# Performance work log

Measured on AMD Instinct MI355X. Metric: run time of the kernel, lower is better.

Reference implementation:

```python
import jax, jax.numpy as jnp
import numpy as np

NUM_LAYERS = 2
VOCAB = 32000
IN_FEAT = 256          # embedding dim is IN_FEAT-1, +1 for cue scalar
HIDDEN = 256
ATN = 64               # hardcoded atn_feature_size in GraphConvolution
CLASSES = 2
B, N = 8, 2048


def setup_inputs() -> dict:
    key = jax.random.key(0)
    ks = jax.random.split(key, 12)
    x = jax.random.randint(ks[0], (B, N), 0, VOCAB, dtype=jnp.int32)
    cue = jax.random.randint(ks[1], (B, N), 0, 2, dtype=jnp.int32)
    adj = (jax.random.uniform(ks[2], (B, N, N)) < 0.01).astype(jnp.float32)
    s = 1.0 / np.sqrt(HIDDEN)
    emb_table = jax.random.normal(ks[3], (VOCAB, IN_FEAT - 1), jnp.float32) * 0.02
    Wh = jax.random.uniform(ks[4], (IN_FEAT, HIDDEN), jnp.float32, -s, s)
    bh = jax.random.uniform(ks[5], (HIDDEN,), jnp.float32, -s, s)
    Wq = jax.random.uniform(ks[6], (HIDDEN, ATN), jnp.float32, -s, s)
    Wk = jax.random.uniform(ks[7], (HIDDEN, ATN), jnp.float32, -s, s)
    Wv = jax.random.uniform(ks[8], (HIDDEN, HIDDEN), jnp.float32, -s, s)
    gcb = jax.random.uniform(ks[9], (HIDDEN,), jnp.float32, -s, s)
    Wc = jax.random.uniform(ks[10], (HIDDEN, CLASSES), jnp.float32, -s, s)
    bc = jax.random.uniform(ks[11], (CLASSES,), jnp.float32, -s, s)
    return {"x": x, "cue": cue, "adj": adj, "emb_table": emb_table,
            "Wh": Wh, "bh": bh, "Wq": Wq, "Wk": Wk, "Wv": Wv,
            "gcb": gcb, "Wc": Wc, "bc": bc}


def graph_attention_layer(h, adj, Wq, Wk, Wv, gcb):
    # h: [B,N,H]; adj: [B,N,N] binary. Per node i: softmax over neighbors j of
    # (Wk h_j) . (Wq h_i), weighted sum of Wv h_j. Zero-degree nodes get 0 (pre-bias).
    q = jnp.einsum('bnh,ha->bna', h, Wq)        # [B,N,A]
    k = jnp.einsum('bnh,ha->bna', h, Wk)        # [B,N,A]
    v = jnp.einsum('bnh,hg->bng', h, Wv)        # [B,N,H]
    logits = jnp.einsum('bia,bja->bij', q, k)   # [B,N,N]
    mask = adj > 0
    attn = jax.nn.softmax(jnp.where(mask, logits, -1e9), axis=-1)
    out = jnp.einsum('bij,bjh->bih', attn, v)   # [B,N,H]
    has_nbr = jnp.any(mask, axis=-1, keepdims=True)  # [B,N,1]
    return jnp.where(has_nbr, out, 0.0) + gcb


def reference(x, cue, adj, emb_table, Wh, bh, Wq, Wk, Wv, gcb, Wc, bc):
    emb = emb_table[x]                                   # [B,N,IN_FEAT-1]
    feats = jnp.concatenate([emb, cue.astype(jnp.float32)[..., None]], axis=-1)
    h = jax.nn.relu(jnp.einsum('bnf,fh->bnh', feats, Wh) + bh)
    for _ in range(NUM_LAYERS):
        h = jax.nn.sigmoid(graph_attention_layer(h, adj, Wq, Wk, Wv, gcb))
    logits = jnp.einsum('bnh,hc->bnc', h, Wc) + bc
    return jax.nn.softmax(logits, axis=-1)
```

## Files before the change

### kernel.cpp

```cpp
#include <hip/hip_runtime.h>
#include <hip/hip_bf16.h>


#define NB 8
#define NN 2048
#define ROWS (NB * NN)
#define MAXD 64

typedef float f4 __attribute__((ext_vector_type(4)));
typedef _Float16 hf;
typedef _Float16 h2 __attribute__((ext_vector_type(2)));
typedef _Float16 h4 __attribute__((ext_vector_type(4)));
typedef _Float16 h8 __attribute__((ext_vector_type(8)));
typedef unsigned int  u32;
typedef unsigned short u16;

__device__ __forceinline__ float sigmoidf_(float x) { return 1.f / (1.f + __expf(-x)); }
__device__ __forceinline__ h2 u2h(u32 u) { union { u32 u; h2 h; } c; c.u = u; return c.h; }

__device__ __forceinline__ float dot2_(h2 a, h2 b, float c) {
#if __has_builtin(__builtin_amdgcn_fdot2)
    return __builtin_amdgcn_fdot2(a, b, c, false);
#else
    return c + (float)a.x * (float)b.x + (float)a.y * (float)b.y;
#endif
}
__device__ __forceinline__ u32 permlo_(u32 hi, u32 lo) { return __builtin_amdgcn_perm(hi, lo, 0x05040100u); }
__device__ __forceinline__ u32 permhi_(u32 hi, u32 lo) { return __builtin_amdgcn_perm(hi, lo, 0x07060302u); }

#define PACK_BLKS 96
#define EMB_BLKS 512

__global__ __launch_bounds__(256) void k_fused_front(
        const int* __restrict__ x, const int* __restrict__ cue,
        const float* __restrict__ adj, const float* __restrict__ emb,
        const float* __restrict__ Wh, const float* __restrict__ bh,
        const float* __restrict__ Wq, const float* __restrict__ Wk,
        const float* __restrict__ Wv,
        hf* __restrict__ hB, hf* __restrict__ Wpt,
        int* __restrict__ deg, int* __restrict__ nbr) {
    __shared__ float As[32 * 64];
    __shared__ float Ws[32 * 128];
    int bid = blockIdx.x;
    int t = threadIdx.x;

    if (bid < PACK_BLKS) {
        int idxp = bid * 256 + t;
#pragma unroll
        for (int r = 0; r < 4; ++r) {
            int i = idxp + r * PACK_BLKS * 256;
            int c = i >> 8, f = i & 255;
            float v;
            if (c < 64)       v = Wq[f * 64 + c];
            else if (c < 128) v = Wk[f * 64 + (c - 64)];
            else              v = Wv[f * 256 + (c - 128)];
            Wpt[i] = (hf)v;
        }
        return;
    }

    if (bid < PACK_BLKS + EMB_BLKS) {
        int eb = bid - PACK_BLKS;
        int rt = eb >> 1, ct = eb & 1;
        int row0 = rt * 64, col0 = ct * 128;
        int sm = t & 63, skg = t >> 6;
        int swc = (t & 31) * 4, swk = t >> 5;
        int tx = t & 15, ty = t >> 4;
        int xr = x[row0 + sm];
        float cv = (float)cue[row0 + sm];
        const float* er = emb + (size_t)xr * 255;

        float acc[4][8];
#pragma unroll
        for (int i = 0; i < 4; ++i)
#pragma unroll
            for (int j = 0; j < 8; ++j) acc[i][j] = 0.f;

        for (int kc = 0; kc < 256; kc += 32) {
            int kb = skg * 8;
#pragma unroll
            for (int u = 0; u < 8; ++u) {
                int f = kc + kb + u;
                As[(kb + u) * 64 + sm] = (f < 255) ? er[f] : cv;
            }
#pragma unroll
            for (int r = 0; r < 4; ++r) {
                int kk = swk + r * 8;
                f4 w = *(const f4*)(Wh + (size_t)(kc + kk) * 256 + col0 + swc);
                *(f4*)&Ws[kk * 128 + swc] = w;
            }
            __syncthreads();
#pragma unroll
            for (int k = 0; k < 32; ++k) {
                f4 av = *(f4*)&As[k * 64 + ty * 4];
                f4 w0 = *(f4*)&Ws[k * 128 + tx * 8];
                f4 w1 = *(f4*)&Ws[k * 128 + tx * 8 + 4];
                float a[4] = {av.x, av.y, av.z, av.w};
                float w[8] = {w0.x, w0.y, w0.z, w0.w, w1.x, w1.y, w1.z, w1.w};
#pragma unroll
                for (int i = 0; i < 4; ++i)
#pragma unroll
                    for (int j = 0; j < 8; ++j) acc[i][j] += a[i] * w[j];
            }
            __syncthreads();
        }
        f4 b0 = *(const f4*)(bh + col0 + tx * 8);
        f4 b1 = *(const f4*)(bh + col0 + tx * 8 + 4);
        float bb[8] = {b0.x, b0.y, b0.z, b0.w, b1.x, b1.y, b1.z, b1.w};
#pragma unroll
        for (int i = 0; i < 4; ++i) {
            int row = row0 + ty * 4 + i;
            h8 o;
#pragma unroll
            for (int j = 0; j < 8; ++j) o[j] = (hf)fmaxf(acc[i][j] + bb[j], 0.f);
            *(h8*)(hB + (size_t)row * 256 + col0 + tx * 8) = o;
        }
        return;
    }

    int row = bid - (PACK_BLKS + EMB_BLKS);
    const f4* ar4 = (const f4*)(adj + (size_t)row * NN);
    int* cnt = (int*)As;
    if (t == 0) *cnt = 0;
    __syncthreads();
    int* nr = nbr + (size_t)row * MAXD;
#pragma unroll
    for (int it = 0; it < 2; ++it) {
        int idx = it * 256 + t;
        f4 vv = __builtin_nontemporal_load(ar4 + idx);
        if (vv.x > 0.f) { int p = atomicAdd(cnt, 1); if (p < MAXD) nr[p] = idx * 4 + 0; }
        if (vv.y > 0.f) { int p = atomicAdd(cnt, 1); if (p < MAXD) nr[p] = idx * 4 + 1; }
        if (vv.z > 0.f) { int p = atomicAdd(cnt, 1); if (p < MAXD) nr[p] = idx * 4 + 2; }
        if (vv.w > 0.f) { int p = atomicAdd(cnt, 1); if (p < MAXD) nr[p] = idx * 4 + 3; }
    }
    __syncthreads();
    if (t == 0) deg[row] = (*cnt < MAXD) ? *cnt : MAXD;
}

__global__ __launch_bounds__(256) void k_qkv_mfma(const hf* __restrict__ hB,
                                                  const hf* __restrict__ Wpt,
                                                  hf* __restrict__ qkvB) {
    int t = threadIdx.x;
    int col0 = blockIdx.x * 128, row0 = blockIdx.y * 64;
    int wave = t >> 6, lane = t & 63;
    int l16 = lane & 15, quad = lane >> 4;

    f4 acc[4][2];
#pragma unroll
    for (int i = 0; i < 4; ++i) { acc[i][0] = (f4){0,0,0,0}; acc[i][1] = (f4){0,0,0,0}; }

    const hf* a0 = hB + (size_t)(row0 + l16) * 256 + quad * 8;
    const hf* b0 = Wpt + (size_t)(col0 + wave * 32 + l16) * 256 + quad * 8;

#pragma unroll
    for (int kc = 0; kc < 256; kc += 32) {
        h8 afr[4], bfr[2];
#pragma unroll
        for (int mt = 0; mt < 4; ++mt)
            afr[mt] = *(const h8*)(a0 + (size_t)(mt * 16) * 256 + kc);
#pragma unroll
        for (int nt = 0; nt < 2; ++nt)
            bfr[nt] = *(const h8*)(b0 + (size_t)(nt * 16) * 256 + kc);
#pragma unroll
        for (int mt = 0; mt < 4; ++mt)
#pragma unroll
            for (int nt = 0; nt < 2; ++nt)
                acc[mt][nt] = __builtin_amdgcn_mfma_f32_16x16x32_f16(
                    afr[mt], bfr[nt], acc[mt][nt], 0, 0, 0);
    }
#pragma unroll
    for (int mt = 0; mt < 4; ++mt)
#pragma unroll
        for (int nt = 0; nt < 2; ++nt) {
            int c = col0 + (wave * 2 + nt) * 16 + l16;
#pragma unroll
            for (int reg = 0; reg < 4; ++reg) {
                int r = row0 + mt * 16 + quad * 4 + reg;
                qkvB[(size_t)r * 384 + c] = (hf)acc[mt][nt][reg];
            }
        }
}

template <bool WRITE_OUT>
__global__ __launch_bounds__(256) void k_attn(const hf* __restrict__ qkvB,
                                              const int* __restrict__ deg,
                                              const int* __restrict__ nbr,
                                              const float* __restrict__ gcb,
                                              const float* __restrict__ Wc,
                                              const float* __restrict__ bc,
                                              hf* __restrict__ hB,
                                              float* __restrict__ out) {
    int wave = threadIdx.x >> 6;
    int lane = threadIdx.x & 63;
    int bid = blockIdx.x;
    int row = (bid & 7) * NN + (bid >> 3) * 4 + wave;
    int d = deg[row];
    int l16 = lane & 15, quad = lane >> 4;
    f4 g4 = *(const f4*)(gcb + lane * 4);
    float h0, h1, h2v, h3;
    if (d == 0) {
        h0 = sigmoidf_(g4.x); h1 = sigmoidf_(g4.y);
        h2v = sigmoidf_(g4.z); h3 = sigmoidf_(g4.w);
    } else {
        uint2 qq = *(const uint2*)(qkvB + (size_t)row * 384 + l16 * 4);
        h2 q01 = u2h(qq.x), q23 = u2h(qq.y);
        const int* jl = nbr + (size_t)row * MAXD;
        int bbase = row & ~(NN - 1);
        float m = -1e30f, s = 0.f;
        f4 a = {0, 0, 0, 0};
        for (int e = 0; e < d; e += 4) {
            int idx = e + quad;
            int jg = jl[idx < d ? idx : 0];
            const hf* kr = qkvB + (size_t)(bbase + jg) * 384;
            uint2 kq = *(const uint2*)(kr + 64 + l16 * 4);
            float p = dot2_(u2h(kq.x), q01, dot2_(u2h(kq.y), q23, 0.f));
            p += __shfl_xor(p, 1); p += __shfl_xor(p, 2);
            p += __shfl_xor(p, 4); p += __shfl_xor(p, 8);
            if (idx >= d) p = -1e30f;
            float p0 = __shfl(p, 0),  p1 = __shfl(p, 16);
            float p2 = __shfl(p, 32), p3 = __shfl(p, 48);
            int j0 = __shfl(jg, 0),  j1 = __shfl(jg, 16);
            int j2 = __shfl(jg, 32), j3 = __shfl(jg, 48);
            float mx = fmaxf(fmaxf(p0, p1), fmaxf(p2, p3));
            float mn = fmaxf(m, mx);
            float scale = __expf(m - mn);
            float w0 = __expf(p0 - mn), w1 = __expf(p1 - mn);
            float w2 = __expf(p2 - mn), w3 = __expf(p3 - mn);
            s = s * scale + ((w0 + w1) + (w2 + w3));
            h2 w01; w01.x = (hf)w0; w01.y = (hf)w1;
            h2 w23; w23.x = (hf)w2; w23.y = (hf)w3;
            uint2 u0 = *(const uint2*)(qkvB + (size_t)(bbase + j0) * 384 + 128 + lane * 4);
            uint2 u1 = *(const uint2*)(qkvB + (size_t)(bbase + j1) * 384 + 128 + lane * 4);
            uint2 u2v = *(const uint2*)(qkvB + (size_t)(bbase + j2) * 384 + 128 + lane * 4);
            uint2 u3 = *(const uint2*)(qkvB + (size_t)(bbase + j3) * 384 + 128 + lane * 4);
            a.x = dot2_(u2h(permlo_(u1.x, u0.x)), w01,
                  dot2_(u2h(permlo_(u3.x, u2v.x)), w23, a.x * scale));
            a.y = dot2_(u2h(permhi_(u1.x, u0.x)), w01,
                  dot2_(u2h(permhi_(u3.x, u2v.x)), w23, a.y * scale));
            a.z = dot2_(u2h(permlo_(u1.y, u0.y)), w01,
                  dot2_(u2h(permlo_(u3.y, u2v.y)), w23, a.z * scale));
            a.w = dot2_(u2h(permhi_(u1.y, u0.y)), w01,
                  dot2_(u2h(permhi_(u3.y, u2v.y)), w23, a.w * scale));
            m = mn;
        }
        float inv = 1.f / s;
        h0 = sigmoidf_(a.x * inv + g4.x);
        h1 = sigmoidf_(a.y * inv + g4.y);
        h2v = sigmoidf_(a.z * inv + g4.z);
        h3 = sigmoidf_(a.w * inv + g4.w);
    }
    if (!WRITE_OUT) {
        h4 o; o.x = (hf)h0; o.y = (hf)h1; o.z = (hf)h2v; o.w = (hf)h3;
        *(h4*)(hB + (size_t)row * 256 + lane * 4) = o;
    } else {
        f4 wc0 = *(const f4*)(Wc + lane * 8);
        f4 wc1 = *(const f4*)(Wc + lane * 8 + 4);
        float pa = h0 * wc0.x + h1 * wc0.z + h2v * wc1.x + h3 * wc1.z;
        float pb = h0 * wc0.y + h1 * wc0.w + h2v * wc1.y + h3 * wc1.w;
#pragma unroll
        for (int off = 32; off; off >>= 1) {
            pa += __shfl_xor(pa, off);
            pb += __shfl_xor(pb, off);
        }
        if (lane == 0) {
            float l0 = pa + bc[0], l1 = pb + bc[1];
            float mx = fmaxf(l0, l1);
            float e0 = __expf(l0 - mx), e1 = __expf(l1 - mx);
            float inv = 1.f / (e0 + e1);
            out[(size_t)row * 2 + 0] = e0 * inv;
            out[(size_t)row * 2 + 1] = e1 * inv;
        }
    }
}

extern "C" void kernel_launch(void* const* d_in, const int* in_sizes, int n_in,
                              void* d_out, int out_size, void* d_ws, size_t ws_size,
                              hipStream_t stream) {
    const int*   x    = (const int*)d_in[0];
    const int*   cue  = (const int*)d_in[1];
    const float* adj  = (const float*)d_in[2];
    const float* emb  = (const float*)d_in[3];
    const float* Wh   = (const float*)d_in[4];
    const float* bh   = (const float*)d_in[5];
    const float* Wq   = (const float*)d_in[6];
    const float* Wk   = (const float*)d_in[7];
    const float* Wv   = (const float*)d_in[8];
    const float* gcb  = (const float*)d_in[9];
    const float* Wc   = (const float*)d_in[10];
    const float* bc   = (const float*)d_in[11];
    float* out = (float*)d_out;

    char* w = (char*)d_ws;
    hf*  hB   = (hf*)w;   w += (size_t)ROWS * 256 * 2;
    hf*  qkvB = (hf*)w;   w += (size_t)ROWS * 384 * 2;
    hf*  Wpt  = (hf*)w;   w += (size_t)384 * 256 * 2;
    int* deg  = (int*)w;  w += (size_t)ROWS * 4;
    int* nbr  = (int*)w;

    k_fused_front<<<PACK_BLKS + EMB_BLKS + ROWS, 256, 0, stream>>>(
        x, cue, adj, emb, Wh, bh, Wq, Wk, Wv, hB, Wpt, deg, nbr);
    k_qkv_mfma<<<dim3(3, ROWS / 64), 256, 0, stream>>>(hB, Wpt, qkvB);
    k_attn<false><<<ROWS / 4, 256, 0, stream>>>(qkvB, deg, nbr, gcb, Wc, bc, hB, out);
    k_qkv_mfma<<<dim3(3, ROWS / 64), 256, 0, stream>>>(hB, Wpt, qkvB);
    k_attn<true><<<ROWS / 4, 256, 0, stream>>>(qkvB, deg, nbr, gcb, Wc, bc, hB, out);
}
```

Baseline: 340.0 us.

## Split CSR build across front and QKV kernels, stage QKV GEMM via LDS, batch attention gathers

Measured after the change: 352.6 us. +3.7%, slower.

```diff
diff --git a/kernel.cpp b/kernel.cpp
--- a/kernel.cpp
+++ b/kernel.cpp
@@ -6,19 +6,20 @@
 #define NN 2048
 #define ROWS (NB * NN)
 #define MAXD 64
+#define CSR1 6144
 
 typedef float f4 __attribute__((ext_vector_type(4)));
 typedef _Float16 hf;
-typedef _Float16 h2 __attribute__((ext_vector_type(2)));
-typedef _Float16 h4 __attribute__((ext_vector_type(4)));
-typedef _Float16 h8 __attribute__((ext_vector_type(8)));
-typedef unsigned int  u32;
+typedef _Float16 hx2 __attribute__((ext_vector_type(2)));
+typedef _Float16 hx4 __attribute__((ext_vector_type(4)));
+typedef _Float16 hx8 __attribute__((ext_vector_type(8)));
+typedef unsigned int u32;
 typedef unsigned short u16;
+typedef u16 us8 __attribute__((ext_vector_type(8)));
 
 __device__ __forceinline__ float sigmoidf_(float x) { return 1.f / (1.f + __expf(-x)); }
-__device__ __forceinline__ h2 u2h(u32 u) { union { u32 u; h2 h; } c; c.u = u; return c.h; }
-
-__device__ __forceinline__ float dot2_(h2 a, h2 b, float c) {
+__device__ __forceinline__ hx2 u2h(u32 u) { union { u32 u; hx2 h; } c; c.u = u; return c.h; }
+__device__ __forceinline__ float dot2_(hx2 a, hx2 b, float c) {
 #if __has_builtin(__builtin_amdgcn_fdot2)
     return __builtin_amdgcn_fdot2(a, b, c, false);
 #else
@@ -28,10 +29,27 @@
 __device__ __forceinline__ u32 permlo_(u32 hi, u32 lo) { return __builtin_amdgcn_perm(hi, lo, 0x05040100u); }
 __device__ __forceinline__ u32 permhi_(u32 hi, u32 lo) { return __builtin_amdgcn_perm(hi, lo, 0x07060302u); }
 
-#define PACK_BLKS 96
-#define EMB_BLKS 512
-
-__global__ __launch_bounds__(256) void k_fused_front(
+__device__ __forceinline__ void csr_row(const float* __restrict__ adj,
+                                        int* __restrict__ deg, int* __restrict__ nbr,
+                                        int row, int t, int* cnt) {
+    const f4* ar4 = (const f4*)(adj + (size_t)row * NN);
+    if (t == 0) *cnt = 0;
+    __syncthreads();
+    int* nr = nbr + (size_t)row * MAXD;
+#pragma unroll
+    for (int it = 0; it < 2; ++it) {
+        int idx = it * 256 + t;
+        f4 vv = __builtin_nontemporal_load(ar4 + idx);
+        if (vv.x > 0.f) { int p = atomicAdd(cnt, 1); if (p < MAXD) nr[p] = idx * 4 + 0; }
+        if (vv.y > 0.f) { int p = atomicAdd(cnt, 1); if (p < MAXD) nr[p] = idx * 4 + 1; }
+        if (vv.z > 0.f) { int p = atomicAdd(cnt, 1); if (p < MAXD) nr[p] = idx * 4 + 2; }
+        if (vv.w > 0.f) { int p = atomicAdd(cnt, 1); if (p < MAXD) nr[p] = idx * 4 + 3; }
+    }
+    __syncthreads();
+    if (t == 0) deg[row] = (*cnt < MAXD) ? *cnt : MAXD;
+}
+
+__global__ __launch_bounds__(256) void k_front1(
         const int* __restrict__ x, const int* __restrict__ cue,
         const float* __restrict__ adj, const float* __restrict__ emb,
         const float* __restrict__ Wh, const float* __restrict__ bh,
@@ -44,11 +62,68 @@
     int bid = blockIdx.x;
     int t = threadIdx.x;
 
-    if (bid < PACK_BLKS) {
-        int idxp = bid * 256 + t;
+    if (bid < 512) {
+        int row0 = (bid >> 1) * 64, col0 = (bid & 1) * 128;
+        int srow = t & 63, skg = t >> 6;
+        int swc = (t & 31) * 4, swk = t >> 5;
+        int tx = t & 15, ty = t >> 4;
+        int xr = x[row0 + srow];
+        float cv = (float)cue[row0 + srow];
+        const float* er = emb + (size_t)xr * 255;
+
+        float acc[4][8];
+#pragma unroll
+        for (int i = 0; i < 4; ++i)
+#pragma unroll
+            for (int j = 0; j < 8; ++j) acc[i][j] = 0.f;
+
+        for (int kc = 0; kc < 256; kc += 32) {
+            int kb = skg * 8;
+#pragma unroll
+            for (int u = 0; u < 8; ++u) {
+                int f = kc + kb + u;
+                As[(kb + u) * 64 + srow] = (f < 255) ? er[f] : cv;
+            }
+#pragma unroll
+            for (int r = 0; r < 4; ++r) {
+                int kk = swk + r * 8;
+                f4 w = *(const f4*)(Wh + (size_t)(kc + kk) * 256 + col0 + swc);
+                *(f4*)&Ws[kk * 128 + swc] = w;
+            }
+            __syncthreads();
+#pragma unroll
+            for (int k = 0; k < 32; ++k) {
+                f4 av = *(f4*)&As[k * 64 + ty * 4];
+                f4 w0 = *(f4*)&Ws[k * 128 + tx * 8];
+                f4 w1 = *(f4*)&Ws[k * 128 + tx * 8 + 4];
+                float a[4] = {av.x, av.y, av.z, av.w};
+                float w[8] = {w0.x, w0.y, w0.z, w0.w, w1.x, w1.y, w1.z, w1.w};
+#pragma unroll
+                for (int i = 0; i < 4; ++i)
+#pragma unroll
+                    for (int j = 0; j < 8; ++j) acc[i][j] += a[i] * w[j];
+            }
+            __syncthreads();
+        }
+        f4 b0 = *(const f4*)(bh + col0 + tx * 8);
+        f4 b1 = *(const f4*)(bh + col0 + tx * 8 + 4);
+        float bb[8] = {b0.x, b0.y, b0.z, b0.w, b1.x, b1.y, b1.z, b1.w};
+#pragma unroll
+        for (int i = 0; i < 4; ++i) {
+            int row = row0 + ty * 4 + i;
+            hx8 o;
+#pragma unroll
+            for (int j = 0; j < 8; ++j) o[j] = (hf)fmaxf(acc[i][j] + bb[j], 0.f);
+            *(hx8*)(hB + (size_t)row * 256 + col0 + tx * 8) = o;
+        }
+        return;
+    }
+
+    if (bid < 608) {
+        int base = (bid - 512) * 256 + t;
 #pragma unroll
         for (int r = 0; r < 4; ++r) {
-            int i = idxp + r * PACK_BLKS * 256;
+            int i = base + r * 96 * 256;
             int c = i >> 8, f = i & 255;
             float v;
             if (c < 64)       v = Wq[f * 64 + c];
@@ -59,108 +134,45 @@
         return;
     }
 
-    if (bid < PACK_BLKS + EMB_BLKS) {
-        int eb = bid - PACK_BLKS;
-        int rt = eb >> 1, ct = eb & 1;
-        int row0 = rt * 64, col0 = ct * 128;
-        int sm = t & 63, skg = t >> 6;
-        int swc = (t & 31) * 4, swk = t >> 5;
-        int tx = t & 15, ty = t >> 4;
-        int xr = x[row0 + sm];
-        float cv = (float)cue[row0 + sm];
-        const float* er = emb + (size_t)xr * 255;
-
-        float acc[4][8];
-#pragma unroll
-        for (int i = 0; i < 4; ++i)
-#pragma unroll
-            for (int j = 0; j < 8; ++j) acc[i][j] = 0.f;
-
-        for (int kc = 0; kc < 256; kc += 32) {
-            int kb = skg * 8;
-#pragma unroll
-            for (int u = 0; u < 8; ++u) {
-                int f = kc + kb + u;
-                As[(kb + u) * 64 + sm] = (f < 255) ? er[f] : cv;
-            }
-#pragma unroll
-            for (int r = 0; r < 4; ++r) {
-                int kk = swk + r * 8;
-                f4 w = *(const f4*)(Wh + (size_t)(kc + kk) * 256 + col0 + swc);
-                *(f4*)&Ws[kk * 128 + swc] = w;
-            }
-            __syncthreads();
-#pragma unroll
-            for (int k = 0; k < 32; ++k) {
-                f4 av = *(f4*)&As[k * 64 + ty * 4];
-                f4 w0 = *(f4*)&Ws[k * 128 + tx * 8];
-                f4 w1 = *(f4*)&Ws[k * 128 + tx * 8 + 4];
-                float a[4] = {av.x, av.y, av.z, av.w};
-                float w[8] = {w0.x, w0.y, w0.z, w0.w, w1.x, w1.y, w1.z, w1.w};
-#pragma unroll
-                for (int i = 0; i < 4; ++i)
-#pragma unroll
-                    for (int j = 0; j < 8; ++j) acc[i][j] += a[i] * w[j];
-            }
-            __syncthreads();
-        }
-        f4 b0 = *(const f4*)(bh + col0 + tx * 8);
-        f4 b1 = *(const f4*)(bh + col0 + tx * 8 + 4);
-        float bb[8] = {b0.x, b0.y, b0.z, b0.w, b1.x, b1.y, b1.z, b1.w};
-#pragma unroll
-        for (int i = 0; i < 4; ++i) {
-            int row = row0 + ty * 4 + i;
-            h8 o;
-#pragma unroll
-            for (int j = 0; j < 8; ++j) o[j] = (hf)fmaxf(acc[i][j] + bb[j], 0.f);
-            *(h8*)(hB + (size_t)row * 256 + col0 + tx * 8) = o;
-        }
-        return;
-    }
-
-    int row = bid - (PACK_BLKS + EMB_BLKS);
-    const f4* ar4 = (const f4*)(adj + (size_t)row * NN);
-    int* cnt = (int*)As;
-    if (t == 0) *cnt = 0;
-    __syncthreads();
-    int* nr = nbr + (size_t)row * MAXD;
-#pragma unroll
-    for (int it = 0; it < 2; ++it) {
-        int idx = it * 256 + t;
-        f4 vv = __builtin_nontemporal_load(ar4 + idx);
-        if (vv.x > 0.f) { int p = atomicAdd(cnt, 1); if (p < MAXD) nr[p] = idx * 4 + 0; }
-        if (vv.y > 0.f) { int p = atomicAdd(cnt, 1); if (p < MAXD) nr[p] = idx * 4 + 1; }
-        if (vv.z > 0.f) { int p = atomicAdd(cnt, 1); if (p < MAXD) nr[p] = idx * 4 + 2; }
-        if (vv.w > 0.f) { int p = atomicAdd(cnt, 1); if (p < MAXD) nr[p] = idx * 4 + 3; }
-    }
-    __syncthreads();
-    if (t == 0) deg[row] = (*cnt < MAXD) ? *cnt : MAXD;
-}
-
-__global__ __launch_bounds__(256) void k_qkv_mfma(const hf* __restrict__ hB,
-                                                  const hf* __restrict__ Wpt,
-                                                  hf* __restrict__ qkvB) {
-    int t = threadIdx.x;
-    int col0 = blockIdx.x * 128, row0 = blockIdx.y * 64;
+    csr_row(adj, deg, nbr, bid - 608, t, (int*)As);
+}
+
+union QSMem {
+    struct { u16 As[64 * 40]; u16 Bs[128 * 40]; } q;
+    int cnt;
+};
+
+__device__ __forceinline__ void qkv_tile(const hf* __restrict__ hB,
+                                         const hf* __restrict__ Wpt,
+                                         hf* __restrict__ qkvB,
+                                         int tile, int t, QSMem& sm) {
+    int col0 = (tile % 3) * 128, row0 = (tile / 3) * 64;
     int wave = t >> 6, lane = t & 63;
     int l16 = lane & 15, quad = lane >> 4;
-
     f4 acc[4][2];
 #pragma unroll
     for (int i = 0; i < 4; ++i) { acc[i][0] = (f4){0,0,0,0}; acc[i][1] = (f4){0,0,0,0}; }
-
-    const hf* a0 = hB + (size_t)(row0 + l16) * 256 + quad * 8;
-    const hf* b0 = Wpt + (size_t)(col0 + wave * 32 + l16) * 256 + quad * 8;
-
-#pragma unroll
+    int ar = t >> 2, ao = (t & 3) * 8;
+    int bcs = t >> 1, bo = (t & 1) * 16;
+    const u16* hB16 = (const u16*)hB;
+    const u16* Wp16 = (const u16*)Wpt;
+
     for (int kc = 0; kc < 256; kc += 32) {
-        h8 afr[4], bfr[2];
+        us8 av  = *(const us8*)(hB16 + (size_t)(row0 + ar) * 256 + kc + ao);
+        us8 bv0 = *(const us8*)(Wp16 + (size_t)(col0 + bcs) * 256 + kc + bo);
+        us8 bv1 = *(const us8*)(Wp16 + (size_t)(col0 + bcs) * 256 + kc + bo + 8);
+        __syncthreads();
+        *(us8*)&sm.q.As[ar * 40 + ao] = av;
+        *(us8*)&sm.q.Bs[bcs * 40 + bo] = bv0;
+        *(us8*)&sm.q.Bs[bcs * 40 + bo + 8] = bv1;
+        __syncthreads();
+        hx8 afr[4], bfr[2];
 #pragma unroll
         for (int mt = 0; mt < 4; ++mt)
-            afr[mt] = *(const h8*)(a0 + (size_t)(mt * 16) * 256 + kc);
+            afr[mt] = *(hx8*)&sm.q.As[(mt * 16 + l16) * 40 + quad * 8];
 #pragma unroll
         for (int nt = 0; nt < 2; ++nt)
-            bfr[nt] = *(const h8*)(b0 + (size_t)(nt * 16) * 256 + kc);
+            bfr[nt] = *(hx8*)&sm.q.Bs[((wave * 2 + nt) * 16 + l16) * 40 + quad * 8];
 #pragma unroll
         for (int mt = 0; mt < 4; ++mt)
 #pragma unroll
@@ -179,6 +191,25 @@
                 qkvB[(size_t)r * 384 + c] = (hf)acc[mt][nt][reg];
             }
         }
+}
+
+__global__ __launch_bounds__(256) void k_qkv_csr(const hf* __restrict__ hB,
+                                                 const hf* __restrict__ Wpt,
+                                                 hf* __restrict__ qkvB,
+                                                 const float* __restrict__ adj,
+                                                 int* __restrict__ deg,
+                                                 int* __restrict__ nbr) {
+    __shared__ QSMem sm;
+    int bid = blockIdx.x, t = threadIdx.x;
+    if (bid < 768) qkv_tile(hB, Wpt, qkvB, bid, t, sm);
+    else           csr_row(adj, deg, nbr, CSR1 + (bid - 768), t, &sm.cnt);
+}
+
+__global__ __launch_bounds__(256) void k_qkv(const hf* __restrict__ hB,
+                                             const hf* __restrict__ Wpt,
+                                             hf* __restrict__ qkvB) {
+    __shared__ QSMem sm;
+    qkv_tile(hB, Wpt, qkvB, blockIdx.x, threadIdx.x, sm);
 }
 
 template <bool WRITE_OUT>
@@ -197,66 +228,93 @@
     int d = deg[row];
     int l16 = lane & 15, quad = lane >> 4;
     f4 g4 = *(const f4*)(gcb + lane * 4);
-    float h0, h1, h2v, h3;
+    float h0, h1, h2c, h3;
     if (d == 0) {
         h0 = sigmoidf_(g4.x); h1 = sigmoidf_(g4.y);
-        h2v = sigmoidf_(g4.z); h3 = sigmoidf_(g4.w);
+        h2c = sigmoidf_(g4.z); h3 = sigmoidf_(g4.w);
     } else {
         uint2 qq = *(const uint2*)(qkvB + (size_t)row * 384 + l16 * 4);
-        h2 q01 = u2h(qq.x), q23 = u2h(qq.y);
-        const int* jl = nbr + (size_t)row * MAXD;
+        hx2 q01 = u2h(qq.x), q23 = u2h(qq.y);
+        int jlane = nbr[(size_t)row * MAXD + lane];
         int bbase = row & ~(NN - 1);
         float m = -1e30f, s = 0.f;
         f4 a = {0, 0, 0, 0};
-        for (int e = 0; e < d; e += 4) {
-            int idx = e + quad;
-            int jg = jl[idx < d ? idx : 0];
-            const hf* kr = qkvB + (size_t)(bbase + jg) * 384;
-            uint2 kq = *(const uint2*)(kr + 64 + l16 * 4);
-            float p = dot2_(u2h(kq.x), q01, dot2_(u2h(kq.y), q23, 0.f));
-            p += __shfl_xor(p, 1); p += __shfl_xor(p, 2);
-            p += __shfl_xor(p, 4); p += __shfl_xor(p, 8);
-            if (idx >= d) p = -1e30f;
-            float p0 = __shfl(p, 0),  p1 = __shfl(p, 16);
-            float p2 = __shfl(p, 32), p3 = __shfl(p, 48);
-            int j0 = __shfl(jg, 0),  j1 = __shfl(jg, 16);
-            int j2 = __shfl(jg, 32), j3 = __shfl(jg, 48);
-            float mx = fmaxf(fmaxf(p0, p1), fmaxf(p2, p3));
-            float mn = fmaxf(m, mx);
-            float scale = __expf(m - mn);
-            float w0 = __expf(p0 - mn), w1 = __expf(p1 - mn);
-            float w2 = __expf(p2 - mn), w3 = __expf(p3 - mn);
-            s = s * scale + ((w0 + w1) + (w2 + w3));
-            h2 w01; w01.x = (hf)w0; w01.y = (hf)w1;
-            h2 w23; w23.x = (hf)w2; w23.y = (hf)w3;
-            uint2 u0 = *(const uint2*)(qkvB + (size_t)(bbase + j0) * 384 + 128 + lane * 4);
-            uint2 u1 = *(const uint2*)(qkvB + (size_t)(bbase + j1) * 384 + 128 + lane * 4);
-            uint2 u2v = *(const uint2*)(qkvB + (size_t)(bbase + j2) * 384 + 128 + lane * 4);
-            uint2 u3 = *(const uint2*)(qkvB + (size_t)(bbase + j3) * 384 + 128 + lane * 4);
-            a.x = dot2_(u2h(permlo_(u1.x, u0.x)), w01,
-                  dot2_(u2h(permlo_(u3.x, u2v.x)), w23, a.x * scale));
-            a.y = dot2_(u2h(permhi_(u1.x, u0.x)), w01,
-                  dot2_(u2h(permhi_(u3.x, u2v.x)), w23, a.y * scale));
-            a.z = dot2_(u2h(permlo_(u1.y, u0.y)), w01,
-                  dot2_(u2h(permlo_(u3.y, u2v.y)), w23, a.z * scale));
-            a.w = dot2_(u2h(permhi_(u1.y, u0.y)), w01,
-                  dot2_(u2h(permhi_(u3.y, u2v.y)), w23, a.w * scale));
+        for (int e0 = 0; e0 < d; e0 += 16) {
+            int jr[4]; uint2 kqr[4]; uint2 vr[4][4];
+#pragma unroll
+            for (int g = 0; g < 4; ++g) {
+                if (e0 + g * 4 < d) {
+                    int idx = e0 + g * 4 + quad;
+                    jr[g] = __shfl(jlane, idx < d ? idx : 0);
+                    kqr[g] = *(const uint2*)(qkvB + (size_t)(bbase + jr[g]) * 384 + 64 + l16 * 4);
+                }
+            }
+#pragma unroll
+            for (int g = 0; g < 4; ++g) {
+                if (e0 + g * 4 < d) {
+                    int j0 = __shfl(jr[g], 0),  j1 = __shfl(jr[g], 16);
+                    int j2 = __shfl(jr[g], 32), j3 = __shfl(jr[g], 48);
+                    vr[g][0] = *(const uint2*)(qkvB + (size_t)(bbase + j0) * 384 + 128 + lane * 4);
+                    vr[g][1] = *(const uint2*)(qkvB + (size_t)(bbase + j1) * 384 + 128 + lane * 4);
+                    vr[g][2] = *(const uint2*)(qkvB + (size_t)(bbase + j2) * 384 + 128 + lane * 4);
+                    vr[g][3] = *(const uint2*)(qkvB + (size_t)(bbase + j3) * 384 + 128 + lane * 4);
+                }
+            }
+            float pg[4];
+#pragma unroll
+            for (int g = 0; g < 4; ++g) {
+                if (e0 + g * 4 < d) {
+                    float p = dot2_(u2h(kqr[g].x), q01, dot2_(u2h(kqr[g].y), q23, 0.f));
+                    p += __shfl_xor(p, 1); p += __shfl_xor(p, 2);
+                    p += __shfl_xor(p, 4); p += __shfl_xor(p, 8);
+                    int idx = e0 + g * 4 + quad;
+                    pg[g] = (idx < d) ? p : -1e30f;
+                } else pg[g] = -1e30f;
+            }
+            float cm = fmaxf(fmaxf(pg[0], pg[1]), fmaxf(pg[2], pg[3]));
+            cm = fmaxf(cm, __shfl_xor(cm, 16));
+            cm = fmaxf(cm, __shfl_xor(cm, 32));
+            float mn = fmaxf(m, cm);
+            float sc = __expf(m - mn);
+            s *= sc; a.x *= sc; a.y *= sc; a.z *= sc; a.w *= sc;
             m = mn;
+#pragma unroll
+            for (int g = 0; g < 4; ++g) {
+                if (e0 + g * 4 < d) {
+                    float w = __expf(pg[g] - mn);
+                    float sw = w + __shfl_xor(w, 16);
+                    sw = sw + __shfl_xor(sw, 32);
+                    s += sw;
+                    float w0 = __shfl(w, 0),  w1 = __shfl(w, 16);
+                    float w2 = __shfl(w, 32), w3 = __shfl(w, 48);
+                    hx2 w01, w23;
+                    w01.x = (hf)w0; w01.y = (hf)w1;
+                    w23.x = (hf)w2; w23.y = (hf)w3;
+                    a.x = dot2_(u2h(permlo_(vr[g][1].x, vr[g][0].x)), w01,
+                          dot2_(u2h(permlo_(vr[g][3].x, vr[g][2].x)), w23, a.x));
+                    a.y = dot2_(u2h(permhi_(vr[g][1].x, vr[g][0].x)), w01,
+                          dot2_(u2h(permhi_(vr[g][3].x, vr[g][2].x)), w23, a.y));
+                    a.z = dot2_(u2h(permlo_(vr[g][1].y, vr[g][0].y)), w01,
+                          dot2_(u2h(permlo_(vr[g][3].y, vr[g][2].y)), w23, a.z));
+                    a.w = dot2_(u2h(permhi_(vr[g][1].y, vr[g][0].y)), w01,
+                          dot2_(u2h(permhi_(vr[g][3].y, vr[g][2].y)), w23, a.w));
+                }
+            }
         }
         float inv = 1.f / s;
         h0 = sigmoidf_(a.x * inv + g4.x);
         h1 = sigmoidf_(a.y * inv + g4.y);
-        h2v = sigmoidf_(a.z * inv + g4.z);
+        h2c = sigmoidf_(a.z * inv + g4.z);
         h3 = sigmoidf_(a.w * inv + g4.w);
     }
     if (!WRITE_OUT) {
-        h4 o; o.x = (hf)h0; o.y = (hf)h1; o.z = (hf)h2v; o.w = (hf)h3;
-        *(h4*)(hB + (size_t)row * 256 + lane * 4) = o;
+        hx4 o; o.x = (hf)h0; o.y = (hf)h1; o.z = (hf)h2c; o.w = (hf)h3;
+        *(hx4*)(hB + (size_t)row * 256 + lane * 4) = o;
     } else {
         f4 wc0 = *(const f4*)(Wc + lane * 8);
         f4 wc1 = *(const f4*)(Wc + lane * 8 + 4);
-        float pa = h0 * wc0.x + h1 * wc0.z + h2v * wc1.x + h3 * wc1.z;
-        float pb = h0 * wc0.y + h1 * wc0.w + h2v * wc1.y + h3 * wc1.w;
+        float pa = h0 * wc0.x + h1 * wc0.z + h2c * wc1.x + h3 * wc1.z;
+        float pb = h0 * wc0.y + h1 * wc0.w + h2c * wc1.y + h3 * wc1.w;
 #pragma unroll
         for (int off = 32; off; off >>= 1) {
             pa += __shfl_xor(pa, off);
@@ -266,9 +324,9 @@
             float l0 = pa + bc[0], l1 = pb + bc[1];
             float mx = fmaxf(l0, l1);
             float e0 = __expf(l0 - mx), e1 = __expf(l1 - mx);
-            float inv = 1.f / (e0 + e1);
-            out[(size_t)row * 2 + 0] = e0 * inv;
-            out[(size_t)row * 2 + 1] = e1 * inv;
+            float inv2 = 1.f / (e0 + e1);
+            out[(size_t)row * 2 + 0] = e0 * inv2;
+            out[(size_t)row * 2 + 1] = e1 * inv2;
         }
     }
 }
@@ -297,10 +355,10 @@
     int* deg  = (int*)w;  w += (size_t)ROWS * 4;
     int* nbr  = (int*)w;
 
-    k_fused_front<<<PACK_BLKS + EMB_BLKS + ROWS, 256, 0, stream>>>(
+    k_front1<<<608 + CSR1, 256, 0, stream>>>(
         x, cue, adj, emb, Wh, bh, Wq, Wk, Wv, hB, Wpt, deg, nbr);
-    k_qkv_mfma<<<dim3(3, ROWS / 64), 256, 0, stream>>>(hB, Wpt, qkvB);
+    k_qkv_csr<<<768 + (ROWS - CSR1), 256, 0, stream>>>(hB, Wpt, qkvB, adj, deg, nbr);
     k_attn<false><<<ROWS / 4, 256, 0, stream>>>(qkvB, deg, nbr, gcb, Wc, bc, hB, out);
-    k_qkv_mfma<<<dim3(3, ROWS / 64), 256, 0, stream>>>(hB, Wpt, qkvB);
+    k_qkv<<<768, 256, 0, stream>>>(hB, Wpt, qkvB);
     k_attn<true><<<ROWS / 4, 256, 0, stream>>>(qkvB, deg, nbr, gcb, Wc, bc, hB, out);
 }
```
